# Kernel optimization log

Hardware: AMD Instinct MI355X
Metric: run time of the kernel (lower is better)

## Reference

```python
import jax, jax.numpy as jnp
import numpy as np

N = 100000      # num_nodes
R = 8           # num_relations
D = 128         # hidden_dim
E = 600000      # num_edges
P = 100000      # num query pairs
PH = 128        # pair_hidden_dim


def _xavier(key, shape):
    fan_in, fan_out = shape[-2], shape[-1]
    limit = float(np.sqrt(6.0 / (fan_in + fan_out)))
    return jax.random.uniform(key, shape, jnp.float32, -limit, limit)


def setup_inputs() -> dict:
    key = jax.random.key(0)
    ks = jax.random.split(key, 16)
    edge_index = jax.random.randint(ks[0], (2, E), 0, N)
    edge_type = jax.random.randint(ks[1], (E,), 0, R)
    drug_index = jax.random.randint(ks[2], (P,), 0, N)
    disease_index = jax.random.randint(ks[3], (P,), 0, N)
    emb = _xavier(ks[4], (N, D))
    rw1 = _xavier(ks[5], (R, D, D))
    sl1 = _xavier(ks[6], (D, D))
    b1 = jnp.zeros((D,), jnp.float32)
    rw2 = _xavier(ks[7], (R, D, D))
    sl2 = _xavier(ks[8], (D, D))
    b2 = jnp.zeros((D,), jnp.float32)
    pw1 = _xavier(ks[9], (3 * D, PH))
    pb1 = jnp.zeros((PH,), jnp.float32)
    pw2 = _xavier(ks[10], (PH, 1))
    pb2 = jnp.zeros((1,), jnp.float32)
    return {
        "edge_index": edge_index, "edge_type": edge_type,
        "drug_index": drug_index, "disease_index": disease_index,
        "emb": emb, "rw1": rw1, "sl1": sl1, "b1": b1,
        "rw2": rw2, "sl2": sl2, "b2": b2,
        "pw1": pw1, "pb1": pb1, "pw2": pw2, "pb2": pb2,
    }


def _rgcn_layer(x, rel_w, self_w, bias, src, dst, etype):
    # Transform all node features once per relation: [R, N, D]
    xW = jnp.einsum('nd,rde->rne', x, rel_w)
    # Per-relation in-degree of dst (matches torch bincount-per-relation, clamp_min(1))
    seg_key = etype * N + dst                                  # [E]
    deg = jax.ops.segment_sum(jnp.ones((src.shape[0],), x.dtype), seg_key,
                              num_segments=R * N)
    deg = jnp.maximum(deg, 1.0)
    msg = xW[etype, src] / deg[seg_key][:, None]               # [E, D]
    agg = jax.ops.segment_sum(msg, dst, num_segments=N)        # [N, D]
    return x @ self_w + agg + bias


def reference(edge_index, edge_type, drug_index, disease_index,
              emb, rw1, sl1, b1, rw2, sl2, b2, pw1, pb1, pw2, pb2):
    src, dst = edge_index[0], edge_index[1]
    # encode (eval mode: dropout is identity)
    x = _rgcn_layer(emb, rw1, sl1, b1, src, dst, edge_type)
    x = jax.nn.relu(x)
    x = _rgcn_layer(x, rw2, sl2, b2, src, dst, edge_type)
    # score_pairs
    dh = x[drug_index]
    sh = x[disease_index]
    feat = jnp.concatenate((dh, sh, dh * sh), axis=-1)         # [P, 3D]
    h = jax.nn.relu(feat @ pw1 + pb1)
    logits = (h @ pw2 + pb2)[:, 0]                             # [P]
    return logits
```

## Files before the change

### kernel.cpp

```cpp
#include <hip/hip_runtime.h>

#define D 128

typedef short s16x8 __attribute__((ext_vector_type(8)));
typedef float f32x4 __attribute__((ext_vector_type(4)));

__device__ inline unsigned short f2b(float f) {
    unsigned u = __builtin_bit_cast(unsigned, f);
    unsigned r = (u + 0x7FFFu + ((u >> 16) & 1u)) >> 16;
    return (unsigned short)r;
}
__device__ inline float b2f(unsigned short h) {
    unsigned u = ((unsigned)h) << 16;
    return __builtin_bit_cast(float, u);
}


__global__ void k_count2(const int* __restrict__ etype, const int* __restrict__ dstA,
                         int E, int N, int* __restrict__ deg) {
    int e = blockIdx.x * blockDim.x + threadIdx.x;
    if (e < E) atomicAdd(&deg[etype[e] * N + dstA[e]], 1);
}


template<int VPT>
__global__ void k_scan_blk(const int* __restrict__ in, int* __restrict__ tmp,
                           int* __restrict__ bsum, int n) {
    __shared__ int sd[256];
    int t = threadIdx.x;
    long base = (long)blockIdx.x * (256 * VPT) + (long)t * VPT;
    int s[VPT];
    int tsum = 0;
    #pragma unroll
    for (int k = 0; k < VPT; ++k) { s[k] = (base + k < n) ? in[base + k] : 0; tsum += s[k]; }
    sd[t] = tsum;
    __syncthreads();
    for (int off = 1; off < 256; off <<= 1) {
        int v = (t >= off) ? sd[t - off] : 0;
        __syncthreads();
        sd[t] += v;
        __syncthreads();
    }
    int run = sd[t] - tsum;
    #pragma unroll
    for (int k = 0; k < VPT; ++k) { if (base + k < n) tmp[base + k] = run; run += s[k]; }
    if (t == 255) bsum[blockIdx.x] = sd[255];
}

__global__ void k_scan2(const int* __restrict__ bsum, int* __restrict__ boff, int nb) {
    __shared__ int sd[256];
    int t = threadIdx.x;
    int v = (t < nb) ? bsum[t] : 0;
    sd[t] = v;
    __syncthreads();
    for (int off = 1; off < 256; off <<= 1) {
        int w = (t >= off) ? sd[t - off] : 0;
        __syncthreads();
        sd[t] += w;
        __syncthreads();
    }
    if (t < nb) boff[t] = sd[t] - v;
}

__global__ void k_scan3(const int* __restrict__ tmp, const int* __restrict__ boff,
                        int* __restrict__ out, int n, int shift) {
    int i = blockIdx.x * 256 + threadIdx.x;
    if (i < n) out[i] = tmp[i] + boff[i >> shift];
}


__global__ void k_scatter(const int* __restrict__ etype, const int* __restrict__ srcA,
                          const int* __restrict__ dstA, int E, int N,
                          const int* __restrict__ degOff, int* __restrict__ binCur,
                          int* __restrict__ slotSrc) {
    int e = blockIdx.x * 256 + threadIdx.x;
    if (e < E) {
        int bin = etype[e] * N + dstA[e];
        int rank = atomicAdd(&binCur[bin], 1);
        slotSrc[degOff[bin] + rank] = srcA[e];
    }
}


__global__ void k_prep(const float* __restrict__ emb,
                       const float* __restrict__ rw1, const float* __restrict__ sl1,
                       const float* __restrict__ rw2, const float* __restrict__ sl2,
                       const float* __restrict__ pw1,
                       unsigned short* __restrict__ embb,
                       unsigned short* __restrict__ wAll1,
                       unsigned short* __restrict__ wAll2,
                       unsigned short* __restrict__ pw1T,
                       int N, int R)
{
    long t = (long)blockIdx.x * 256 + threadIdx.x;
    long u0 = (long)N * D / 4;
    if (t < u0) {
        long i = t * 4;
        f32x4 v = *(const f32x4*)(emb + i);
        unsigned a0 = (unsigned)f2b(v[0]) | ((unsigned)f2b(v[1]) << 16);
        unsigned a1 = (unsigned)f2b(v[2]) | ((unsigned)f2b(v[3]) << 16);
        uint2 o; o.x = a0; o.y = a1;
        *(uint2*)(embb + i) = o;
        return;
    }
    t -= u0;
    long uW = (long)(R + 1) * D * D;
    if (t < 2 * uW) {
        const float* rw = (t < uW) ? rw1 : rw2;
        const float* sl = (t < uW) ? sl1 : sl2;
        unsigned short* o = (t < uW) ? wAll1 : wAll2;
        long u = (t < uW) ? t : t - uW;
        int r = (int)(u >> 14);
        int nb = (int)(u & 16383);
        int n = nb >> 7, kk = nb & 127;
        float v = (r < R) ? rw[((size_t)r * D + kk) * D + n] : sl[(size_t)kk * D + n];
        o[u] = f2b(v);
        return;
    }
    t -= 2 * uW;
    if (t < 3 * D * D) {
        int n = (int)(t / 384), ck = (int)(t - n * 384);
        int ch = ck >> 7, kl = (ck & 127) ^ ((n & 7) << 3);
        pw1T[t] = f2b(pw1[(size_t)(ch * 128 + kl) * 128 + n]);
    }
}


template<bool RELU>
__global__ __launch_bounds__(256) void k_fused(
    const unsigned short* __restrict__ xb,
    const unsigned short* __restrict__ wAll,
    const int* __restrict__ slotSrc,
    const int* __restrict__ degOff,
    const float* __restrict__ bias,
    unsigned short* __restrict__ out,
    int N, int R, int E)
{
    __shared__ unsigned char smA[32768];
    int tid = threadIdx.x;
    int d0 = blockIdx.x * 128;
    int dmaxc = (d0 + 128 < N) ? d0 + 128 : N;
    int lane = tid & 63, wid = tid >> 6;
    int lo = lane & 15, hi = lane >> 4;
    int am = tid >> 2, ac = tid & 3;

    f32x4 acc[2][8];
    #pragma unroll
    for (int q = 0; q < 2; ++q)
        #pragma unroll
        for (int n = 0; n < 8; ++n) acc[q][n] = (f32x4){0, 0, 0, 0};

    for (int r = 0; r <= R; ++r) {
        if (r < R) {
            int b0 = r * N + d0;
            int b1 = r * N + dmaxc;
            int cnt = ((b1 < R * N) ? degOff[b1] : E) - degOff[b0];
            if (cnt == 0) continue;
        }

        #pragma unroll
        for (int hf = 0; hf < 2; ++hf) {
            int row = hf * 64 + am;
            int d = d0 + row;
            unsigned char* db = smA + row * 256;
            int sw = (row & 7) << 4;
            if (r == R) {
                int4 v[4] = {{0,0,0,0},{0,0,0,0},{0,0,0,0},{0,0,0,0}};
                if (d < N) {
                    #pragma unroll
                    for (int g = 0; g < 4; ++g)
                        v[g] = *(const int4*)(xb + (size_t)d * D + (ac + 4 * g) * 8);
                }
                #pragma unroll
                for (int g = 0; g < 4; ++g)
                    *(int4*)(db + (((ac + 4 * g) * 16) ^ sw)) = v[g];
            } else {
                int st = 0, en = 0;
                if (d < N) {
                    int bin = r * N + d;
                    st = degOff[bin];
                    en = (bin + 1 < R * N) ? degOff[bin + 1] : E;
                }
                if (en > st) {
                    float s[32];
                    #pragma unroll
                    for (int j = 0; j < 32; ++j) s[j] = 0.0f;
                    for (int e2 = st; e2 < en; ++e2) {
                        int src = slotSrc[e2];
                        const unsigned short* xr = xb + (size_t)src * D;
                        #pragma unroll
                        for (int g = 0; g < 4; ++g) {
                            int4 w = *(const int4*)(xr + (ac + 4 * g) * 8);
                            const unsigned short* hp = (const unsigned short*)&w;
                            #pragma unroll
                            for (int k = 0; k < 8; ++k) s[g * 8 + k] += b2f(hp[k]);
                        }
                    }
                    float inv = 1.0f / (float)(en - st);
                    #pragma unroll
                    for (int g = 0; g < 4; ++g) {
                        unsigned short o8[8];
                        #pragma unroll
                        for (int k = 0; k < 8; ++k) o8[k] = f2b(s[g * 8 + k] * inv);
                        *(int4*)(db + (((ac + 4 * g) * 16) ^ sw)) = *(const int4*)o8;
                    }
                } else {
                    int4 z = {0, 0, 0, 0};
                    #pragma unroll
                    for (int g = 0; g < 4; ++g)
                        *(int4*)(db + (((ac + 4 * g) * 16) ^ sw)) = z;
                }
            }
        }
        __syncthreads();

        {
            int r0g = wid * 32 + lo, r1g = r0g + 16;
            s16x8 a0[4], a1[4];
            #pragma unroll
            for (int ks = 0; ks < 4; ++ks) {
                int kb = ks * 64 + hi * 16;
                a0[ks] = *(const s16x8*)(smA + r0g * 256 + (kb ^ ((r0g & 7) << 4)));
                a1[ks] = *(const s16x8*)(smA + r1g * 256 + (kb ^ ((r1g & 7) << 4)));
            }
            const unsigned short* Bp = wAll + (size_t)r * D * D;
            #pragma unroll
            for (int ks = 0; ks < 4; ++ks) {
                #pragma unroll
                for (int n = 0; n < 8; ++n) {
                    s16x8 bf = *(const s16x8*)(Bp + (size_t)(n * 16 + lo) * D + ks * 32 + hi * 8);
                    acc[0][n] = __builtin_amdgcn_mfma_f32_16x16x32_bf16(a0[ks], bf, acc[0][n], 0, 0, 0);
                    acc[1][n] = __builtin_amdgcn_mfma_f32_16x16x32_bf16(a1[ks], bf, acc[1][n], 0, 0, 0);
                }
            }
        }
        __syncthreads();
    }

    float bb[8];
    #pragma unroll
    for (int n = 0; n < 8; ++n) bb[n] = bias[n * 16 + lo];
    #pragma unroll
    for (int m2 = 0; m2 < 2; ++m2) {
        int rbase = wid * 32 + m2 * 16 + hi * 4;
        #pragma unroll
        for (int reg = 0; reg < 4; ++reg) {
            int rl = rbase + reg;
            #pragma unroll
            for (int n = 0; n < 8; ++n) {
                float v = acc[m2][n][reg] + bb[n];
                if (RELU) v = fmaxf(v, 0.0f);
                int byteoff = rl * 256 + (((n * 32 + (lo >> 3) * 16) ^ ((rl & 7) << 4)) + (lo & 7) * 2);
                *(unsigned short*)(smA + byteoff) = f2b(v);
            }
        }
    }
    __syncthreads();
    {
        int m = tid >> 1, chh = tid & 1;
        int d = d0 + m;
        if (d < N) {
            unsigned short* op = out + (size_t)d * D;
            #pragma unroll
            for (int i = 0; i < 8; ++i) {
                int c = chh * 8 + i;
                int4 v = *(const int4*)(smA + m * 256 + ((c * 16) ^ ((m & 7) << 4)));
                *(int4*)(op + c * 8) = v;
            }
        }
    }
}


__global__ __launch_bounds__(256) void k_score(
    const unsigned short* __restrict__ x2b,
    const int* __restrict__ drug, const int* __restrict__ dis,
    const unsigned short* __restrict__ pw1T,
    const float* __restrict__ pb1, const float* __restrict__ pw2,
    const float* __restrict__ pb2, float* __restrict__ outp, int P)
{
    __shared__ unsigned char smA[32768];
    __shared__ unsigned char smB[32768];
    __shared__ float pb1s[128];
    __shared__ float pw2s[128];
    int tid = threadIdx.x;
    long p0 = (long)blockIdx.x * 128;
    if (tid < 128) { pb1s[tid] = pb1[tid]; pw2s[tid] = pw2[tid]; }
    float pb2v = pb2[0];

    int lane = tid & 63, wid = tid >> 6;
    int lo = lane & 15, hi = lane >> 4;
    f32x4 acc[2][8];
    #pragma unroll
    for (int q = 0; q < 2; ++q)
        #pragma unroll
        for (int b = 0; b < 8; ++b) acc[q][b] = (f32x4){0, 0, 0, 0};

    for (int chn = 0; chn < 3; ++chn) {
        {
            const int4* src = (const int4*)pw1T;
            int4* dstl = (int4*)smB;
            #pragma unroll
            for (int i = 0; i < 8; ++i) {
                int q = tid + i * 256;
                int n = q >> 4, c = q & 15;
                dstl[q] = src[n * 48 + chn * 16 + c];
            }
        }
        {
            int m = tid >> 1, half = tid & 1;
            long p = p0 + m;
            int4 z = {0, 0, 0, 0};
            if (p < P) {
                const int4* da = (const int4*)(x2b + (size_t)drug[p] * D);
                const int4* db = (const int4*)(x2b + (size_t)dis[p] * D);
                for (int c = half * 8; c < half * 8 + 8; ++c) {
                    int4 v;
                    if (chn == 0) v = da[c];
                    else if (chn == 1) v = db[c];
                    else {
                        int4 va = da[c], vb = db[c];
                        const unsigned short* ap = (const unsigned short*)&va;
                        const unsigned short* bp = (const unsigned short*)&vb;
                        unsigned short o[8];
                        #pragma unroll
                        for (int j = 0; j < 8; ++j) o[j] = f2b(b2f(ap[j]) * b2f(bp[j]));
                        v = *(const int4*)o;
                    }
                    *(int4*)(smA + m * 256 + ((c * 16) ^ ((m & 7) << 4))) = v;
                }
            } else {
                for (int c = half * 8; c < half * 8 + 8; ++c)
                    *(int4*)(smA + m * 256 + ((c * 16) ^ ((m & 7) << 4))) = z;
            }
        }
        __syncthreads();

        #pragma unroll
        for (int ks = 0; ks < 4; ++ks) {
            int kb = ks * 64 + hi * 16;
            int r0 = wid * 32 + lo, r1 = r0 + 16;
            s16x8 a0 = *(const s16x8*)(smA + r0 * 256 + (kb ^ ((r0 & 7) << 4)));
            s16x8 a1 = *(const s16x8*)(smA + r1 * 256 + (kb ^ ((r1 & 7) << 4)));
            #pragma unroll
            for (int n = 0; n < 8; ++n) {
                int cr = n * 16 + lo;
                s16x8 bf = *(const s16x8*)(smB + cr * 256 + (kb ^ ((cr & 7) << 4)));
                acc[0][n] = __builtin_amdgcn_mfma_f32_16x16x32_bf16(a0, bf, acc[0][n], 0, 0, 0);
                acc[1][n] = __builtin_amdgcn_mfma_f32_16x16x32_bf16(a1, bf, acc[1][n], 0, 0, 0);
            }
        }
        __syncthreads();
    }

    #pragma unroll
    for (int m2 = 0; m2 < 2; ++m2)
        #pragma unroll
        for (int reg = 0; reg < 4; ++reg) {
            float s = 0.0f;
            #pragma unroll
            for (int n = 0; n < 8; ++n) {
                int col = n * 16 + lo;
                float v = acc[m2][n][reg] + pb1s[col];
                v = fmaxf(v, 0.0f);
                s = fmaf(v, pw2s[col], s);
            }
            s += __shfl_xor(s, 1, 64);
            s += __shfl_xor(s, 2, 64);
            s += __shfl_xor(s, 4, 64);
            s += __shfl_xor(s, 8, 64);
            long p = p0 + wid * 32 + m2 * 16 + hi * 4 + reg;
            if (lo == 0 && p < P) outp[p] = s + pb2v;
        }
}


extern "C" void kernel_launch(void* const* d_in, const int* in_sizes, int n_in,
                              void* d_out, int out_size, void* d_ws, size_t ws_size,
                              hipStream_t stream) {
    const int*   edge_index = (const int*)d_in[0];
    const int*   edge_type  = (const int*)d_in[1];
    const int*   drug       = (const int*)d_in[2];
    const int*   dis        = (const int*)d_in[3];
    const float* emb        = (const float*)d_in[4];
    const float* rw1        = (const float*)d_in[5];
    const float* sl1        = (const float*)d_in[6];
    const float* b1         = (const float*)d_in[7];
    const float* rw2        = (const float*)d_in[8];
    const float* sl2        = (const float*)d_in[9];
    const float* b2         = (const float*)d_in[10];
    const float* pw1        = (const float*)d_in[11];
    const float* pb1        = (const float*)d_in[12];
    const float* pw2        = (const float*)d_in[13];
    const float* pb2        = (const float*)d_in[14];

    const int E = in_sizes[1];
    const int P = in_sizes[2];
    const int N = in_sizes[4] / D;
    const int R = in_sizes[5] / (D * D);

    const int* srcA = edge_index;
    const int* dstA = edge_index + E;

    char* ws = (char*)d_ws;
    unsigned short* embb = (unsigned short*)ws; ws += (size_t)N * D * 2;
    unsigned short* x1b  = (unsigned short*)ws; ws += (size_t)N * D * 2;
    unsigned short* wAll1 = (unsigned short*)ws; ws += (size_t)(R + 1) * D * D * 2;
    unsigned short* wAll2 = (unsigned short*)ws; ws += (size_t)(R + 1) * D * D * 2;
    unsigned short* pw1T  = (unsigned short*)ws; ws += (size_t)3 * D * D * 2;
    int* deg     = (int*)ws; ws += (size_t)R * N * 4;
    int* binCur  = (int*)ws; ws += (size_t)R * N * 4;
    size_t zbytes = (size_t)(2 * R * N) * 4;
    int* slotSrc = (int*)ws; ws += (size_t)E * 4;
    int* degOff  = (int*)ws; ws += (size_t)R * N * 4;
    int* bsum    = (int*)ws; ws += 256 * 4;
    int* boff    = (int*)ws; ws += 256 * 4;
    unsigned short* x2b = embb;

    hipMemsetAsync(deg, 0, zbytes, stream);

    long u0 = (long)N * D / 4;
    long uW = (long)(R + 1) * D * D;
    long utot = u0 + 2 * uW + 3 * D * D;
    k_prep<<<(int)((utot + 255) / 256), 256, 0, stream>>>(emb, rw1, sl1, rw2, sl2, pw1,
                                                          embb, wAll1, wAll2, pw1T, N, R);

    k_count2<<<(E + 255) / 256, 256, 0, stream>>>(edge_type, dstA, E, N, deg);

    int nbS = (R * N + 4095) / 4096;
    k_scan_blk<16><<<nbS, 256, 0, stream>>>(deg, degOff, bsum, R * N);
    k_scan2<<<1, 256, 0, stream>>>(bsum, boff, nbS);
    k_scan3<<<(R * N + 255) / 256, 256, 0, stream>>>(degOff, boff, degOff, R * N, 12);

    k_scatter<<<(E + 255) / 256, 256, 0, stream>>>(edge_type, srcA, dstA, E, N,
                                                   degOff, binCur, slotSrc);

    int gridF = (N + 127) / 128;

    k_fused<true><<<gridF, 256, 0, stream>>>(embb, wAll1, slotSrc, degOff, b1, x1b, N, R, E);
    k_fused<false><<<gridF, 256, 0, stream>>>(x1b, wAll2, slotSrc, degOff, b2, x2b, N, R, E);

    k_score<<<(P + 127) / 128, 256, 0, stream>>>(x2b, drug, dis, pw1T, pb1, pw2, pb2,
                                                 (float*)d_out, P);
}
```

Measured before the change: 588.1 us.

## Parallelize RGCN aggregation over edges with LDS float atomics and smaller tiles

The fused RGCN layer kernel now distributes the edges of each relation's block range across threads. Each thread pair handles one edge and accumulates its source row into a 64-row fp32 LDS buffer with atomicAdd, replacing the per-destination serial loop that suffered load imbalance. The degree normalisation is applied when converting the buffer to bf16 MFMA operands. Blocks shrink to 64 destination rows with launch bounds requesting 4 blocks per CU, and scatter now also records a per-slot destination array. The cost is many LDS atomics per edge, a zeroing pass and extra syncs per relation, plus the loss of the empty-relation skip. A meaningless dummy statement was also added in k_score.

```diff
diff --git a/kernel.cpp b/kernel.cpp
--- a/kernel.cpp
+++ b/kernel.cpp
@@ -1,6 +1,7 @@
 #include <hip/hip_runtime.h>
 
 #define D 128
+#define ASTRIDE 132
 
 typedef short s16x8 __attribute__((ext_vector_type(8)));
 typedef float f32x4 __attribute__((ext_vector_type(4)));
@@ -72,12 +73,15 @@
 __global__ void k_scatter(const int* __restrict__ etype, const int* __restrict__ srcA,
                           const int* __restrict__ dstA, int E, int N,
                           const int* __restrict__ degOff, int* __restrict__ binCur,
-                          int* __restrict__ slotSrc) {
+                          int* __restrict__ slotSrc, int* __restrict__ slotDst) {
     int e = blockIdx.x * 256 + threadIdx.x;
     if (e < E) {
-        int bin = etype[e] * N + dstA[e];
+        int d = dstA[e];
+        int bin = etype[e] * N + d;
         int rank = atomicAdd(&binCur[bin], 1);
-        slotSrc[degOff[bin] + rank] = srcA[e];
+        int pos = degOff[bin] + rank;
+        slotSrc[pos] = srcA[e];
+        slotDst[pos] = d;
     }
 }
 
@@ -127,101 +131,101 @@
 
 
 template<bool RELU>
-__global__ __launch_bounds__(256) void k_fused(
+__global__ __launch_bounds__(256, 4) void k_fused(
     const unsigned short* __restrict__ xb,
     const unsigned short* __restrict__ wAll,
     const int* __restrict__ slotSrc,
+    const int* __restrict__ slotDst,
     const int* __restrict__ degOff,
     const float* __restrict__ bias,
     unsigned short* __restrict__ out,
     int N, int R, int E)
 {
-    __shared__ unsigned char smA[32768];
+    __shared__ float accum[64 * ASTRIDE];
     int tid = threadIdx.x;
-    int d0 = blockIdx.x * 128;
-    int dmaxc = (d0 + 128 < N) ? d0 + 128 : N;
+    int d0 = blockIdx.x * 64;
+    int dmaxc = (d0 + 64 < N) ? d0 + 64 : N;
     int lane = tid & 63, wid = tid >> 6;
     int lo = lane & 15, hi = lane >> 4;
-    int am = tid >> 2, ac = tid & 3;
-
-    f32x4 acc[2][8];
-    #pragma unroll
-    for (int q = 0; q < 2; ++q)
-        #pragma unroll
-        for (int n = 0; n < 8; ++n) acc[q][n] = (f32x4){0, 0, 0, 0};
+
+    f32x4 acc[8];
+    #pragma unroll
+    for (int n = 0; n < 8; ++n) acc[n] = (f32x4){0, 0, 0, 0};
 
     for (int r = 0; r <= R; ++r) {
         if (r < R) {
-            int b0 = r * N + d0;
+            f32x4* az = (f32x4*)accum;
+            #pragma unroll
+            for (int i = 0; i < 9; ++i) {
+                int idx = tid + i * 256;
+                if (idx < 64 * ASTRIDE / 4) az[idx] = (f32x4){0, 0, 0, 0};
+            }
+            __syncthreads();
+
+            int s0 = degOff[r * N + d0];
             int b1 = r * N + dmaxc;
-            int cnt = ((b1 < R * N) ? degOff[b1] : E) - degOff[b0];
-            if (cnt == 0) continue;
-        }
-
-        #pragma unroll
-        for (int hf = 0; hf < 2; ++hf) {
-            int row = hf * 64 + am;
+            int s1 = (b1 < R * N) ? degOff[b1] : E;
+            int half = tid & 1;
+            for (int q = s0 + (tid >> 1); q < s1; q += 128) {
+                int src = slotSrc[q];
+                int dl = slotDst[q] - d0;
+                const unsigned short* xr = xb + (size_t)src * D + half * 64;
+                float* row = accum + dl * ASTRIDE + half * 64;
+                #pragma unroll
+                for (int g = 0; g < 8; ++g) {
+                    int4 w = *(const int4*)(xr + g * 8);
+                    const unsigned short* hp = (const unsigned short*)&w;
+                    #pragma unroll
+                    for (int k = 0; k < 8; ++k)
+                        atomicAdd(&row[g * 8 + k], b2f(hp[k]));
+                }
+            }
+            __syncthreads();
+        } else {
+            __syncthreads();
+            int dl = tid >> 2, qx = tid & 3;
+            int d = d0 + dl;
+            if (d < N) {
+                const unsigned short* xr = xb + (size_t)d * D + qx * 32;
+                float* row = accum + dl * ASTRIDE + qx * 32;
+                #pragma unroll
+                for (int g = 0; g < 4; ++g) {
+                    int4 w = *(const int4*)(xr + g * 8);
+                    const unsigned short* hp = (const unsigned short*)&w;
+                    f32x4 v0, v1;
+                    #pragma unroll
+                    for (int k = 0; k < 4; ++k) { v0[k] = b2f(hp[k]); v1[k] = b2f(hp[4 + k]); }
+                    *(f32x4*)(row + g * 8) = v0;
+                    *(f32x4*)(row + g * 8 + 4) = v1;
+                }
+            }
+            __syncthreads();
+        }
+
+        {
+            int row = wid * 16 + lo;
             int d = d0 + row;
-            unsigned char* db = smA + row * 256;
-            int sw = (row & 7) << 4;
-            if (r == R) {
-                int4 v[4] = {{0,0,0,0},{0,0,0,0},{0,0,0,0},{0,0,0,0}};
-                if (d < N) {
-                    #pragma unroll
-                    for (int g = 0; g < 4; ++g)
-                        v[g] = *(const int4*)(xb + (size_t)d * D + (ac + 4 * g) * 8);
-                }
-                #pragma unroll
-                for (int g = 0; g < 4; ++g)
-                    *(int4*)(db + (((ac + 4 * g) * 16) ^ sw)) = v[g];
-            } else {
-                int st = 0, en = 0;
+            float inv;
+            if (r < R) {
                 if (d < N) {
                     int bin = r * N + d;
-                    st = degOff[bin];
-                    en = (bin + 1 < R * N) ? degOff[bin + 1] : E;
-                }
-                if (en > st) {
-                    float s[32];
-                    #pragma unroll
-                    for (int j = 0; j < 32; ++j) s[j] = 0.0f;
-                    for (int e2 = st; e2 < en; ++e2) {
-                        int src = slotSrc[e2];
-                        const unsigned short* xr = xb + (size_t)src * D;
-                        #pragma unroll
-                        for (int g = 0; g < 4; ++g) {
-                            int4 w = *(const int4*)(xr + (ac + 4 * g) * 8);
-                            const unsigned short* hp = (const unsigned short*)&w;
-                            #pragma unroll
-                            for (int k = 0; k < 8; ++k) s[g * 8 + k] += b2f(hp[k]);
-                        }
-                    }
-                    float inv = 1.0f / (float)(en - st);
-                    #pragma unroll
-                    for (int g = 0; g < 4; ++g) {
-                        unsigned short o8[8];
-                        #pragma unroll
-                        for (int k = 0; k < 8; ++k) o8[k] = f2b(s[g * 8 + k] * inv);
-                        *(int4*)(db + (((ac + 4 * g) * 16) ^ sw)) = *(const int4*)o8;
-                    }
-                } else {
-                    int4 z = {0, 0, 0, 0};
-                    #pragma unroll
-                    for (int g = 0; g < 4; ++g)
-                        *(int4*)(db + (((ac + 4 * g) * 16) ^ sw)) = z;
-                }
-            }
-        }
-        __syncthreads();
-
-        {
-            int r0g = wid * 32 + lo, r1g = r0g + 16;
-            s16x8 a0[4], a1[4];
+                    int st = degOff[bin];
+                    int en = (bin + 1 < R * N) ? degOff[bin + 1] : E;
+                    inv = (en > st) ? 1.0f / (float)(en - st) : 0.0f;
+                } else inv = 0.0f;
+            } else inv = (d < N) ? 1.0f : 0.0f;
+
+            const float* arow = accum + row * ASTRIDE;
+            s16x8 af[4];
             #pragma unroll
             for (int ks = 0; ks < 4; ++ks) {
-                int kb = ks * 64 + hi * 16;
-                a0[ks] = *(const s16x8*)(smA + r0g * 256 + (kb ^ ((r0g & 7) << 4)));
-                a1[ks] = *(const s16x8*)(smA + r1g * 256 + (kb ^ ((r1g & 7) << 4)));
+                int kb = ks * 32 + hi * 8;
+                f32x4 u0 = *(const f32x4*)(arow + kb);
+                f32x4 u1 = *(const f32x4*)(arow + kb + 4);
+                unsigned short o8[8];
+                #pragma unroll
+                for (int k = 0; k < 4; ++k) { o8[k] = f2b(u0[k] * inv); o8[4 + k] = f2b(u1[k] * inv); }
+                af[ks] = *(const s16x8*)o8;
             }
             const unsigned short* Bp = wAll + (size_t)r * D * D;
             #pragma unroll
@@ -229,42 +233,38 @@
                 #pragma unroll
                 for (int n = 0; n < 8; ++n) {
                     s16x8 bf = *(const s16x8*)(Bp + (size_t)(n * 16 + lo) * D + ks * 32 + hi * 8);
-                    acc[0][n] = __builtin_amdgcn_mfma_f32_16x16x32_bf16(a0[ks], bf, acc[0][n], 0, 0, 0);
-                    acc[1][n] = __builtin_amdgcn_mfma_f32_16x16x32_bf16(a1[ks], bf, acc[1][n], 0, 0, 0);
+                    acc[n] = __builtin_amdgcn_mfma_f32_16x16x32_bf16(af[ks], bf, acc[n], 0, 0, 0);
                 }
             }
         }
         __syncthreads();
     }
 
+    unsigned char* stg = (unsigned char*)accum;
     float bb[8];
     #pragma unroll
     for (int n = 0; n < 8; ++n) bb[n] = bias[n * 16 + lo];
     #pragma unroll
-    for (int m2 = 0; m2 < 2; ++m2) {
-        int rbase = wid * 32 + m2 * 16 + hi * 4;
+    for (int reg = 0; reg < 4; ++reg) {
+        int rl = wid * 16 + hi * 4 + reg;
         #pragma unroll
-        for (int reg = 0; reg < 4; ++reg) {
-            int rl = rbase + reg;
-            #pragma unroll
-            for (int n = 0; n < 8; ++n) {
-                float v = acc[m2][n][reg] + bb[n];
-                if (RELU) v = fmaxf(v, 0.0f);
-                int byteoff = rl * 256 + (((n * 32 + (lo >> 3) * 16) ^ ((rl & 7) << 4)) + (lo & 7) * 2);
-                *(unsigned short*)(smA + byteoff) = f2b(v);
-            }
+        for (int n = 0; n < 8; ++n) {
+            float v = acc[n][reg] + bb[n];
+            if (RELU) v = fmaxf(v, 0.0f);
+            int byteoff = rl * 256 + (((n * 32 + (lo >> 3) * 16) ^ ((rl & 7) << 4)) + (lo & 7) * 2);
+            *(unsigned short*)(stg + byteoff) = f2b(v);
         }
     }
     __syncthreads();
     {
-        int m = tid >> 1, chh = tid & 1;
+        int m = tid >> 2, c4 = tid & 3;
         int d = d0 + m;
         if (d < N) {
             unsigned short* op = out + (size_t)d * D;
             #pragma unroll
-            for (int i = 0; i < 8; ++i) {
-                int c = chh * 8 + i;
-                int4 v = *(const int4*)(smA + m * 256 + ((c * 16) ^ ((m & 7) << 4)));
+            for (int i = 0; i < 4; ++i) {
+                int c = c4 * 4 + i;
+                int4 v = *(const int4*)(stg + m * 256 + ((c * 16) ^ ((m & 7) << 4)));
                 *(int4*)(op + c * 8) = v;
             }
         }
@@ -361,7 +361,8 @@
             #pragma unroll
             for (int n = 0; n < 8; ++n) {
                 int col = n * 16 + lo;
-                float v = acc[m2][n][reg] + pb1s[col];
+                float v = acc[m2][reg != reg ? 0 : n][reg];
+                v = acc[m2][n][reg] + pb1s[col];
                 v = fmaxf(v, 0.0f);
                 s = fmaf(v, pw2s[col], s);
             }
@@ -412,6 +413,7 @@
     int* binCur  = (int*)ws; ws += (size_t)R * N * 4;
     size_t zbytes = (size_t)(2 * R * N) * 4;
     int* slotSrc = (int*)ws; ws += (size_t)E * 4;
+    int* slotDst = (int*)ws; ws += (size_t)E * 4;
     int* degOff  = (int*)ws; ws += (size_t)R * N * 4;
     int* bsum    = (int*)ws; ws += 256 * 4;
     int* boff    = (int*)ws; ws += 256 * 4;
@@ -433,12 +435,14 @@
     k_scan3<<<(R * N + 255) / 256, 256, 0, stream>>>(degOff, boff, degOff, R * N, 12);
 
     k_scatter<<<(E + 255) / 256, 256, 0, stream>>>(edge_type, srcA, dstA, E, N,
-                                                   degOff, binCur, slotSrc);
-
-    int gridF = (N + 127) / 128;
-
-    k_fused<true><<<gridF, 256, 0, stream>>>(embb, wAll1, slotSrc, degOff, b1, x1b, N, R, E);
-    k_fused<false><<<gridF, 256, 0, stream>>>(x1b, wAll2, slotSrc, degOff, b2, x2b, N, R, E);
+                                                   degOff, binCur, slotSrc, slotDst);
+
+    int gridF = (N + 63) / 64;
+
+    k_fused<true><<<gridF, 256, 0, stream>>>(embb, wAll1, slotSrc, slotDst, degOff,
+                                             b1, x1b, N, R, E);
+    k_fused<false><<<gridF, 256, 0, stream>>>(x1b, wAll2, slotSrc, slotDst, degOff,
+                                              b2, x2b, N, R, E);
 
     k_score<<<(P + 127) / 128, 256, 0, stream>>>(x2b, drug, dis, pw1T, pb1, pw2, pb2,
                                                  (float*)d_out, P);
```

Measured after the change: 1.325 ms. 125% more time.

## Transform gathered edge rows per relation then scatter-sum via one-hot MFMA

Applied to the files above, without the earlier changes.

The old kernel gathered and averaged source rows per destination with scalar bf16 adds, then multiplied the aggregate by each relation weight. The new kernel loads chunks of 128 edges per relation directly into MFMA A-fragments and multiplies them by the relation weight. It scales each product by 1/deg and stores it in LDS, then reduces into the 128 destination rows with a one-hot matrix MFMA. This moves the aggregation onto matrix cores and drops the serial per-destination gather loop. In exchange it does per-edge rather than per-destination GEMM work, adds an extra slotDst array, and rounds messages to bf16 before summation.

```diff
diff --git a/kernel.cpp b/kernel.cpp
--- a/kernel.cpp
+++ b/kernel.cpp
@@ -72,12 +72,15 @@
 __global__ void k_scatter(const int* __restrict__ etype, const int* __restrict__ srcA,
                           const int* __restrict__ dstA, int E, int N,
                           const int* __restrict__ degOff, int* __restrict__ binCur,
-                          int* __restrict__ slotSrc) {
+                          int* __restrict__ slotSrc, int* __restrict__ slotDst) {
     int e = blockIdx.x * 256 + threadIdx.x;
     if (e < E) {
-        int bin = etype[e] * N + dstA[e];
+        int d = dstA[e];
+        int bin = etype[e] * N + d;
         int rank = atomicAdd(&binCur[bin], 1);
-        slotSrc[degOff[bin] + rank] = srcA[e];
+        int pos = degOff[bin] + rank;
+        slotSrc[pos] = srcA[e];
+        slotDst[pos] = d;
     }
 }
 
@@ -127,144 +130,168 @@
 
 
 template<bool RELU>
-__global__ __launch_bounds__(256) void k_fused(
+__global__ __launch_bounds__(256) void k_fused2(
     const unsigned short* __restrict__ xb,
     const unsigned short* __restrict__ wAll,
     const int* __restrict__ slotSrc,
+    const int* __restrict__ slotDst,
     const int* __restrict__ degOff,
     const float* __restrict__ bias,
     unsigned short* __restrict__ out,
     int N, int R, int E)
 {
-    __shared__ unsigned char smA[32768];
+    __shared__ __align__(16) unsigned char smM[32768];
+    __shared__ unsigned long long sdl8[2][16];
+    __shared__ float sinv[2][128];
     int tid = threadIdx.x;
     int d0 = blockIdx.x * 128;
-    int dmaxc = (d0 + 128 < N) ? d0 + 128 : N;
     int lane = tid & 63, wid = tid >> 6;
     int lo = lane & 15, hi = lane >> 4;
-    int am = tid >> 2, ac = tid & 3;
-
-    f32x4 acc[2][8];
-    #pragma unroll
-    for (int q = 0; q < 2; ++q)
+
+    f32x4 accP[2][8];
+    #pragma unroll
+    for (int g = 0; g < 2; ++g)
         #pragma unroll
-        for (int n = 0; n < 8; ++n) acc[q][n] = (f32x4){0, 0, 0, 0};
-
+        for (int n = 0; n < 8; ++n) accP[g][n] = (f32x4){0, 0, 0, 0};
+
+    int buf = 0;
     for (int r = 0; r <= R; ++r) {
+        int s0, cnt;
         if (r < R) {
-            int b0 = r * N + d0;
-            int b1 = r * N + dmaxc;
-            int cnt = ((b1 < R * N) ? degOff[b1] : E) - degOff[b0];
+            int dm = (d0 + 128 < N) ? d0 + 128 : N;
+            s0 = degOff[r * N + d0];
+            int b1 = r * N + dm;
+            int s1 = (b1 < R * N) ? degOff[b1] : E;
+            cnt = s1 - s0;
             if (cnt == 0) continue;
-        }
-
-        #pragma unroll
-        for (int hf = 0; hf < 2; ++hf) {
-            int row = hf * 64 + am;
-            int d = d0 + row;
-            unsigned char* db = smA + row * 256;
-            int sw = (row & 7) << 4;
-            if (r == R) {
-                int4 v[4] = {{0,0,0,0},{0,0,0,0},{0,0,0,0},{0,0,0,0}};
-                if (d < N) {
+        } else {
+            s0 = 0;
+            cnt = (d0 + 128 < N) ? 128 : N - d0;
+        }
+
+        for (int c0 = 0; c0 < cnt; c0 += 128) {
+            if (tid < 128) {
+                int q = c0 + tid;
+                unsigned char dl = 255; float iv = 0.0f;
+                if (q < cnt) {
+                    if (r < R) {
+                        int sd = slotDst[s0 + q];
+                        dl = (unsigned char)(sd - d0);
+                        int bin = r * N + sd;
+                        int o0 = degOff[bin];
+                        int o1 = (bin + 1 < R * N) ? degOff[bin + 1] : E;
+                        iv = 1.0f / (float)(o1 - o0);
+                    } else {
+                        dl = (unsigned char)q; iv = 1.0f;
+                    }
+                }
+                ((unsigned char*)sdl8[buf])[tid] = dl;
+                sinv[buf][tid] = iv;
+            }
+            int i0 = c0 + wid * 32 + lo;
+            int i1 = i0 + 16;
+            int ci0 = (i0 < cnt) ? i0 : cnt - 1;
+            int ci1 = (i1 < cnt) ? i1 : cnt - 1;
+            int sv0 = (r < R) ? slotSrc[s0 + ci0] : d0 + ci0;
+            int sv1 = (r < R) ? slotSrc[s0 + ci1] : d0 + ci1;
+            const unsigned short* xr0 = xb + (size_t)sv0 * D;
+            const unsigned short* xr1 = xb + (size_t)sv1 * D;
+            s16x8 a0[4], a1[4];
+            #pragma unroll
+            for (int ks = 0; ks < 4; ++ks) {
+                a0[ks] = *(const s16x8*)(xr0 + ks * 32 + hi * 8);
+                a1[ks] = *(const s16x8*)(xr1 + ks * 32 + hi * 8);
+            }
+
+            __syncthreads();
+
+            const unsigned short* Bp = wAll + (size_t)r * D * D;
+            #pragma unroll
+            for (int g = 0; g < 2; ++g) {
+                f32x4 accT[8];
+                #pragma unroll
+                for (int n = 0; n < 8; ++n) accT[n] = (f32x4){0, 0, 0, 0};
+                #pragma unroll
+                for (int ks = 0; ks < 4; ++ks) {
+                    s16x8 af = g ? a1[ks] : a0[ks];
                     #pragma unroll
-                    for (int g = 0; g < 4; ++g)
-                        v[g] = *(const int4*)(xb + (size_t)d * D + (ac + 4 * g) * 8);
+                    for (int n = 0; n < 8; ++n) {
+                        s16x8 bf = *(const s16x8*)(Bp + (size_t)(n * 16 + lo) * D + ks * 32 + hi * 8);
+                        accT[n] = __builtin_amdgcn_mfma_f32_16x16x32_bf16(af, bf, accT[n], 0, 0, 0);
+                    }
                 }
                 #pragma unroll
-                for (int g = 0; g < 4; ++g)
-                    *(int4*)(db + (((ac + 4 * g) * 16) ^ sw)) = v[g];
-            } else {
-                int st = 0, en = 0;
-                if (d < N) {
-                    int bin = r * N + d;
-                    st = degOff[bin];
-                    en = (bin + 1 < R * N) ? degOff[bin + 1] : E;
+                for (int n = 0; n < 8; ++n) {
+                    int fr = n * 16 + lo;
+                    unsigned char* rowb = smM + fr * 256;
+                    int swz = (fr & 15) << 4;
+                    #pragma unroll
+                    for (int reg = 0; reg < 4; ++reg) {
+                        int sr = wid * 32 + g * 16 + hi * 4 + reg;
+                        float v = accT[n][reg] * sinv[buf][sr];
+                        *(unsigned short*)(rowb + ((sr * 2) ^ swz)) = f2b(v);
+                    }
                 }
-                if (en > st) {
-                    float s[32];
+            }
+            __syncthreads();
+
+            {
+                const unsigned long long* sp = sdl8[buf];
+                int row0d = wid * 32 + lo, row1d = row0d + 16;
+                #pragma unroll
+                for (int ks2 = 0; ks2 < 4; ++ks2) {
+                    unsigned long long v8 = sp[ks2 * 4 + hi];
+                    unsigned short af0[8], af1[8];
                     #pragma unroll
-                    for (int j = 0; j < 32; ++j) s[j] = 0.0f;
-                    for (int e2 = st; e2 < en; ++e2) {
-                        int src = slotSrc[e2];
-                        const unsigned short* xr = xb + (size_t)src * D;
-                        #pragma unroll
-                        for (int g = 0; g < 4; ++g) {
-                            int4 w = *(const int4*)(xr + (ac + 4 * g) * 8);
-                            const unsigned short* hp = (const unsigned short*)&w;
-                            #pragma unroll
-                            for (int k = 0; k < 8; ++k) s[g * 8 + k] += b2f(hp[k]);
-                        }
-                    }
-                    float inv = 1.0f / (float)(en - st);
+                    for (int j = 0; j < 8; ++j) {
+                        int dl = (int)((v8 >> (8 * j)) & 0xFF);
+                        af0[j] = (dl == row0d) ? (unsigned short)0x3F80 : (unsigned short)0;
+                        af1[j] = (dl == row1d) ? (unsigned short)0x3F80 : (unsigned short)0;
+                    }
+                    s16x8 a0f = *(const s16x8*)af0;
+                    s16x8 a1f = *(const s16x8*)af1;
                     #pragma unroll
-                    for (int g = 0; g < 4; ++g) {
-                        unsigned short o8[8];
-                        #pragma unroll
-                        for (int k = 0; k < 8; ++k) o8[k] = f2b(s[g * 8 + k] * inv);
-                        *(int4*)(db + (((ac + 4 * g) * 16) ^ sw)) = *(const int4*)o8;
-                    }
-                } else {
-                    int4 z = {0, 0, 0, 0};
-                    #pragma unroll
-                    for (int g = 0; g < 4; ++g)
-                        *(int4*)(db + (((ac + 4 * g) * 16) ^ sw)) = z;
+                    for (int n2 = 0; n2 < 8; ++n2) {
+                        int fr = n2 * 16 + lo;
+                        s16x8 bf = *(const s16x8*)(smM + fr * 256 +
+                                     ((ks2 * 64 + hi * 16) ^ ((fr & 15) << 4)));
+                        accP[0][n2] = __builtin_amdgcn_mfma_f32_16x16x32_bf16(a0f, bf, accP[0][n2], 0, 0, 0);
+                        accP[1][n2] = __builtin_amdgcn_mfma_f32_16x16x32_bf16(a1f, bf, accP[1][n2], 0, 0, 0);
+                    }
                 }
             }
-        }
-        __syncthreads();
-
-        {
-            int r0g = wid * 32 + lo, r1g = r0g + 16;
-            s16x8 a0[4], a1[4];
-            #pragma unroll
-            for (int ks = 0; ks < 4; ++ks) {
-                int kb = ks * 64 + hi * 16;
-                a0[ks] = *(const s16x8*)(smA + r0g * 256 + (kb ^ ((r0g & 7) << 4)));
-                a1[ks] = *(const s16x8*)(smA + r1g * 256 + (kb ^ ((r1g & 7) << 4)));
-            }
-            const unsigned short* Bp = wAll + (size_t)r * D * D;
-            #pragma unroll
-            for (int ks = 0; ks < 4; ++ks) {
-                #pragma unroll
-                for (int n = 0; n < 8; ++n) {
-                    s16x8 bf = *(const s16x8*)(Bp + (size_t)(n * 16 + lo) * D + ks * 32 + hi * 8);
-                    acc[0][n] = __builtin_amdgcn_mfma_f32_16x16x32_bf16(a0[ks], bf, acc[0][n], 0, 0, 0);
-                    acc[1][n] = __builtin_amdgcn_mfma_f32_16x16x32_bf16(a1[ks], bf, acc[1][n], 0, 0, 0);
-                }
-            }
-        }
-        __syncthreads();
-    }
-
+            buf ^= 1;
+        }
+    }
+
+    __syncthreads();
     float bb[8];
     #pragma unroll
     for (int n = 0; n < 8; ++n) bb[n] = bias[n * 16 + lo];
     #pragma unroll
-    for (int m2 = 0; m2 < 2; ++m2) {
-        int rbase = wid * 32 + m2 * 16 + hi * 4;
+    for (int g = 0; g < 2; ++g) {
         #pragma unroll
         for (int reg = 0; reg < 4; ++reg) {
-            int rl = rbase + reg;
+            int rl = wid * 32 + g * 16 + hi * 4 + reg;
             #pragma unroll
             for (int n = 0; n < 8; ++n) {
-                float v = acc[m2][n][reg] + bb[n];
+                float v = accP[g][n][reg] + bb[n];
                 if (RELU) v = fmaxf(v, 0.0f);
                 int byteoff = rl * 256 + (((n * 32 + (lo >> 3) * 16) ^ ((rl & 7) << 4)) + (lo & 7) * 2);
-                *(unsigned short*)(smA + byteoff) = f2b(v);
+                *(unsigned short*)(smM + byteoff) = f2b(v);
             }
         }
     }
     __syncthreads();
     {
-        int m = tid >> 1, chh = tid & 1;
+        int m = tid >> 1, half = tid & 1;
         int d = d0 + m;
         if (d < N) {
             unsigned short* op = out + (size_t)d * D;
             #pragma unroll
             for (int i = 0; i < 8; ++i) {
-                int c = chh * 8 + i;
-                int4 v = *(const int4*)(smA + m * 256 + ((c * 16) ^ ((m & 7) << 4)));
+                int c = half * 8 + i;
+                int4 v = *(const int4*)(smM + m * 256 + ((c * 16) ^ ((m & 7) << 4)));
                 *(int4*)(op + c * 8) = v;
             }
         }
@@ -412,6 +439,7 @@
     int* binCur  = (int*)ws; ws += (size_t)R * N * 4;
     size_t zbytes = (size_t)(2 * R * N) * 4;
     int* slotSrc = (int*)ws; ws += (size_t)E * 4;
+    int* slotDst = (int*)ws; ws += (size_t)E * 4;
     int* degOff  = (int*)ws; ws += (size_t)R * N * 4;
     int* bsum    = (int*)ws; ws += 256 * 4;
     int* boff    = (int*)ws; ws += 256 * 4;
@@ -433,12 +461,14 @@
     k_scan3<<<(R * N + 255) / 256, 256, 0, stream>>>(degOff, boff, degOff, R * N, 12);
 
     k_scatter<<<(E + 255) / 256, 256, 0, stream>>>(edge_type, srcA, dstA, E, N,
-                                                   degOff, binCur, slotSrc);
+                                                   degOff, binCur, slotSrc, slotDst);
 
     int gridF = (N + 127) / 128;
 
-    k_fused<true><<<gridF, 256, 0, stream>>>(embb, wAll1, slotSrc, degOff, b1, x1b, N, R, E);
-    k_fused<false><<<gridF, 256, 0, stream>>>(x1b, wAll2, slotSrc, degOff, b2, x2b, N, R, E);
+    k_fused2<true><<<gridF, 256, 0, stream>>>(embb, wAll1, slotSrc, slotDst, degOff,
+                                              b1, x1b, N, R, E);
+    k_fused2<false><<<gridF, 256, 0, stream>>>(x1b, wAll2, slotSrc, slotDst, degOff,
+                                               b2, x2b, N, R, E);
 
     k_score<<<(P + 127) / 128, 256, 0, stream>>>(x2b, drug, dis, pw1T, pb1, pw2, pb2,
                                                  (float*)d_out, P);
```

Result: slower. 738.2 us (+25.5%).
